# Performance work log

Measured on AMD Instinct MI355X. Metric: run time of the kernel, lower is better.

## Reference

```python
import jax, jax.numpy as jnp
import numpy as np

H = 4096          # hidden_size
NIN = 17          # RFSIZE*RFSIZE + ADDINPUT + NBACTIONS = 9+4+4
NA = 4            # NBACTIONS


def setup_inputs() -> dict:
    key = jax.random.key(0)
    ks = jax.random.split(key, 12)
    return {
        "x": jax.random.normal(ks[0], (1, NIN), jnp.float32),
        "hidden": 0.1 * jax.random.normal(ks[1], (1, H), jnp.float32),
        "hebb": 0.01 * jax.random.normal(ks[2], (H, H), jnp.float32),
        "i2h_w": 0.1 * jax.random.normal(ks[3], (H, NIN), jnp.float32),
        "i2h_b": 0.1 * jax.random.normal(ks[4], (H,), jnp.float32),
        "w": 0.01 * jax.random.uniform(ks[5], (H, H), jnp.float32),
        "alpha": 0.01 * jax.random.uniform(ks[6], (H, H), jnp.float32),
        "eta": 0.01 * jnp.ones((1,), jnp.float32),
        "h2o_w": 0.1 * jax.random.normal(ks[7], (NA, H), jnp.float32),
        "h2o_b": 0.1 * jax.random.normal(ks[8], (NA,), jnp.float32),
        "h2v_w": 0.1 * jax.random.normal(ks[9], (1, H), jnp.float32),
        "h2v_b": 0.1 * jax.random.normal(ks[10], (1,), jnp.float32),
    }


def reference(x, hidden, hebb, i2h_w, i2h_b, w, alpha, eta, h2o_w, h2o_b, h2v_w, h2v_b):
    # plastic RNN step: h = tanh(i2h(x) + hidden @ (w + alpha*hebb))
    h = jnp.tanh(x @ i2h_w.T + i2h_b + hidden @ (w + alpha * hebb))  # [1,H]
    # Hebbian trace update: (1-eta)*hebb + eta * outer(hidden, h)
    hebb_new = (1.0 - eta) * hebb + eta * (hidden[0][:, None] * h[0][None, :])  # [H,H]
    activout = jax.nn.softmax(h @ h2o_w.T + h2o_b, axis=-1)  # [1,NA]
    valueout = h @ h2v_w.T + h2v_b                           # [1,1]
    return activout, valueout, h, hebb_new
```

## Files before the change

### kernel.cpp

```cpp
#include <hip/hip_runtime.h>

#define HDIM 4096
#define NIN 17
#define NA 4

constexpr int TB = 256;
constexpr int CPT = 4;
constexpr int BXC = HDIM / (TB * CPT);
constexpr int NCHUNK = 256;
constexpr int RPC = HDIM / NCHUNK;

__global__ __launch_bounds__(TB)
void k_matvec(const float* __restrict__ w, const float* __restrict__ alpha,
              const float* __restrict__ hebb, const float* __restrict__ hidden,
              float* __restrict__ partial) {
    const int col0 = (blockIdx.x * TB + threadIdx.x) * CPT;
    const int row0 = blockIdx.y * RPC;
    float4 acc = make_float4(0.f, 0.f, 0.f, 0.f);
#pragma unroll 4
    for (int r = 0; r < RPC; ++r) {
        const int i = row0 + r;
        const size_t off = (size_t)i * HDIM + col0;
        const float hv = hidden[i];
        const float4 wv = *(const float4*)(w + off);
        const float4 av = *(const float4*)(alpha + off);
        const float4 bv = *(const float4*)(hebb + off);
        acc.x += hv * (wv.x + av.x * bv.x);
        acc.y += hv * (wv.y + av.y * bv.y);
        acc.z += hv * (wv.z + av.z * bv.z);
        acc.w += hv * (wv.w + av.w * bv.w);
    }
    *(float4*)(partial + (size_t)blockIdx.y * HDIM + col0) = acc;
}

__global__ __launch_bounds__(256)
void k_hact(const float* __restrict__ partial,
            const float* __restrict__ x, const float* __restrict__ i2h_w,
            const float* __restrict__ i2h_b,
            float* __restrict__ h_f, float* __restrict__ h_out) {
    const int j = blockIdx.x * 256 + threadIdx.x;
    float s = 0.f;
    for (int c = 0; c < NCHUNK; ++c) s += partial[(size_t)c * HDIM + j];
    float z = i2h_b[j] + s;
#pragma unroll
    for (int k = 0; k < NIN; ++k) z += x[k] * i2h_w[j * NIN + k];
    const float h = tanhf(z);
    h_f[j] = h;
    h_out[j] = h;
}

__global__ __launch_bounds__(256)
void k_hebb(const float* __restrict__ hebb, const float* __restrict__ hidden,
            const float* __restrict__ h_f, const float* __restrict__ eta,
            float* __restrict__ hebb_out) {
    const size_t m = ((size_t)blockIdx.x * 256 + threadIdx.x) * 4;
    const float e = eta[0];
    const float om = 1.f - e;
    const int i = (int)(m >> 12);
    const int j = (int)(m & (HDIM - 1));
    const float hv = e * hidden[i];
    const float4 hb = *(const float4*)(hebb + m);
    const float4 hj = *(const float4*)(h_f + j);
    hebb_out[m]     = om * hb.x + hv * hj.x;
    hebb_out[m + 1] = om * hb.y + hv * hj.y;
    hebb_out[m + 2] = om * hb.z + hv * hj.z;
    hebb_out[m + 3] = om * hb.w + hv * hj.w;
}

__global__ __launch_bounds__(256)
void k_heads(const float* __restrict__ h_f,
             const float* __restrict__ h2o_w, const float* __restrict__ h2o_b,
             const float* __restrict__ h2v_w, const float* __restrict__ h2v_b,
             float* __restrict__ out) {
    const int tid = threadIdx.x;
    float acc[NA + 1] = {0.f, 0.f, 0.f, 0.f, 0.f};
    for (int t = 0; t < HDIM / 256; ++t) {
        const int j = t * 256 + tid;
        const float hv = h_f[j];
#pragma unroll
        for (int a = 0; a < NA; ++a) acc[a] += hv * h2o_w[a * HDIM + j];
        acc[NA] += hv * h2v_w[j];
    }
    __shared__ float red[256];
    __shared__ float res[NA + 1];
    for (int a = 0; a < NA + 1; ++a) {
        red[tid] = acc[a];
        __syncthreads();
        for (int sft = 128; sft > 0; sft >>= 1) {
            if (tid < sft) red[tid] += red[tid + sft];
            __syncthreads();
        }
        if (tid == 0) res[a] = red[0];
        __syncthreads();
    }
    if (tid == 0) {
        float o[NA];
        float mx = -1e30f;
        for (int a = 0; a < NA; ++a) { o[a] = res[a] + h2o_b[a]; mx = fmaxf(mx, o[a]); }
        float se = 0.f;
        for (int a = 0; a < NA; ++a) { o[a] = __expf(o[a] - mx); se += o[a]; }
        for (int a = 0; a < NA; ++a) out[a] = o[a] / se;
        out[NA] = res[NA] + h2v_b[0];
    }
}

extern "C" void kernel_launch(void* const* d_in, const int* in_sizes, int n_in,
                              void* d_out, int out_size, void* d_ws, size_t ws_size,
                              hipStream_t stream) {
    const float* x      = (const float*)d_in[0];
    const float* hidden = (const float*)d_in[1];
    const float* hebb   = (const float*)d_in[2];
    const float* i2h_w  = (const float*)d_in[3];
    const float* i2h_b  = (const float*)d_in[4];
    const float* w      = (const float*)d_in[5];
    const float* alpha  = (const float*)d_in[6];
    const float* eta    = (const float*)d_in[7];
    const float* h2o_w  = (const float*)d_in[8];
    const float* h2o_b  = (const float*)d_in[9];
    const float* h2v_w  = (const float*)d_in[10];
    const float* h2v_b  = (const float*)d_in[11];
    float* out = (float*)d_out;

    float* partial = (float*)d_ws;
    float* h_f = partial + (size_t)NCHUNK * HDIM;

    float* h_out    = out + 5;
    float* hebb_out = out + 5 + HDIM;

    k_matvec<<<dim3(BXC, NCHUNK), TB, 0, stream>>>(w, alpha, hebb, hidden, partial);
    k_hact<<<HDIM / 256, 256, 0, stream>>>(partial, x, i2h_w, i2h_b, h_f, h_out);
    k_hebb<<<(int)(((size_t)HDIM * HDIM) / 1024), 256, 0, stream>>>(hebb, hidden, h_f, eta, hebb_out);
    k_heads<<<1, 256, 0, stream>>>(h_f, h2o_w, h2o_b, h2v_w, h2v_b, out);
}
```

Baseline: 270.1 us.

## Replace partial-sum buffer with atomic reduction and fuse heads into activation kernel

The matvec kernel now accumulates column sums straight into a zeroed workspace vector with float atomics, replacing the per-chunk partial buffer and its serial reduction over 256 chunks in k_hact. The chunk count doubles to 512, the inner loop is fully unrolled, and a min-blocks-per-CU launch bound is added. The output heads are computed inside k_hact with wavefront shuffles and atomics, so the single-block heads kernel is replaced by a tiny finish kernel. This trades the write and read of a 4 MB partial buffer for 2M atomic adds plus an extra init launch, and the float summation order becomes nondeterministic.

```diff
diff --git a/kernel.cpp b/kernel.cpp
--- a/kernel.cpp
+++ b/kernel.cpp
@@ -7,17 +7,27 @@
 constexpr int TB = 256;
 constexpr int CPT = 4;
 constexpr int BXC = HDIM / (TB * CPT);
-constexpr int NCHUNK = 256;
+constexpr int NCHUNK = 512;
 constexpr int RPC = HDIM / NCHUNK;
 
-__global__ __launch_bounds__(TB)
+#define WS_Z 0
+#define WS_RES 4096
+#define WS_HF 4104
+
+__global__ __launch_bounds__(256)
+void k_init(float* __restrict__ ws) {
+    const int i = blockIdx.x * 256 + threadIdx.x;
+    if (i < WS_HF) ws[i] = 0.f;
+}
+
+__global__ __launch_bounds__(TB, 4)
 void k_matvec(const float* __restrict__ w, const float* __restrict__ alpha,
               const float* __restrict__ hebb, const float* __restrict__ hidden,
-              float* __restrict__ partial) {
+              float* __restrict__ z) {
     const int col0 = (blockIdx.x * TB + threadIdx.x) * CPT;
     const int row0 = blockIdx.y * RPC;
     float4 acc = make_float4(0.f, 0.f, 0.f, 0.f);
-#pragma unroll 4
+#pragma unroll
     for (int r = 0; r < RPC; ++r) {
         const int i = row0 + r;
         const size_t off = (size_t)i * HDIM + col0;
@@ -30,23 +40,57 @@
         acc.z += hv * (wv.z + av.z * bv.z);
         acc.w += hv * (wv.w + av.w * bv.w);
     }
-    *(float4*)(partial + (size_t)blockIdx.y * HDIM + col0) = acc;
+    atomicAdd(z + col0 + 0, acc.x);
+    atomicAdd(z + col0 + 1, acc.y);
+    atomicAdd(z + col0 + 2, acc.z);
+    atomicAdd(z + col0 + 3, acc.w);
 }
 
 __global__ __launch_bounds__(256)
-void k_hact(const float* __restrict__ partial,
+void k_hact(const float* __restrict__ z,
             const float* __restrict__ x, const float* __restrict__ i2h_w,
             const float* __restrict__ i2h_b,
-            float* __restrict__ h_f, float* __restrict__ h_out) {
+            const float* __restrict__ h2o_w, const float* __restrict__ h2v_w,
+            float* __restrict__ h_f, float* __restrict__ h_out,
+            float* __restrict__ res) {
     const int j = blockIdx.x * 256 + threadIdx.x;
-    float s = 0.f;
-    for (int c = 0; c < NCHUNK; ++c) s += partial[(size_t)c * HDIM + j];
-    float z = i2h_b[j] + s;
+    float zv = z[j] + i2h_b[j];
 #pragma unroll
-    for (int k = 0; k < NIN; ++k) z += x[k] * i2h_w[j * NIN + k];
-    const float h = tanhf(z);
+    for (int k = 0; k < NIN; ++k) zv += x[k] * i2h_w[j * NIN + k];
+    const float h = tanhf(zv);
     h_f[j] = h;
     h_out[j] = h;
+    float d[NA + 1];
+#pragma unroll
+    for (int a = 0; a < NA; ++a) d[a] = h * h2o_w[a * HDIM + j];
+    d[NA] = h * h2v_w[j];
+#pragma unroll
+    for (int a = 0; a < NA + 1; ++a) {
+#pragma unroll
+        for (int off = 32; off > 0; off >>= 1) d[a] += __shfl_down(d[a], off);
+    }
+    if ((threadIdx.x & 63) == 0) {
+#pragma unroll
+        for (int a = 0; a < NA + 1; ++a) atomicAdd(res + a, d[a]);
+    }
+}
+
+__global__ void k_finish(const float* __restrict__ res,
+                         const float* __restrict__ h2o_b,
+                         const float* __restrict__ h2v_b,
+                         float* __restrict__ out) {
+    if (threadIdx.x == 0) {
+        float o[NA];
+        float mx = -1e30f;
+#pragma unroll
+        for (int a = 0; a < NA; ++a) { o[a] = res[a] + h2o_b[a]; mx = fmaxf(mx, o[a]); }
+        float se = 0.f;
+#pragma unroll
+        for (int a = 0; a < NA; ++a) { o[a] = __expf(o[a] - mx); se += o[a]; }
+#pragma unroll
+        for (int a = 0; a < NA; ++a) out[a] = o[a] / se;
+        out[NA] = res[NA] + h2v_b[0];
+    }
 }
 
 __global__ __launch_bounds__(256)
@@ -67,43 +111,6 @@
     hebb_out[m + 3] = om * hb.w + hv * hj.w;
 }
 
-__global__ __launch_bounds__(256)
-void k_heads(const float* __restrict__ h_f,
-             const float* __restrict__ h2o_w, const float* __restrict__ h2o_b,
-             const float* __restrict__ h2v_w, const float* __restrict__ h2v_b,
-             float* __restrict__ out) {
-    const int tid = threadIdx.x;
-    float acc[NA + 1] = {0.f, 0.f, 0.f, 0.f, 0.f};
-    for (int t = 0; t < HDIM / 256; ++t) {
-        const int j = t * 256 + tid;
-        const float hv = h_f[j];
-#pragma unroll
-        for (int a = 0; a < NA; ++a) acc[a] += hv * h2o_w[a * HDIM + j];
-        acc[NA] += hv * h2v_w[j];
-    }
-    __shared__ float red[256];
-    __shared__ float res[NA + 1];
-    for (int a = 0; a < NA + 1; ++a) {
-        red[tid] = acc[a];
-        __syncthreads();
-        for (int sft = 128; sft > 0; sft >>= 1) {
-            if (tid < sft) red[tid] += red[tid + sft];
-            __syncthreads();
-        }
-        if (tid == 0) res[a] = red[0];
-        __syncthreads();
-    }
-    if (tid == 0) {
-        float o[NA];
-        float mx = -1e30f;
-        for (int a = 0; a < NA; ++a) { o[a] = res[a] + h2o_b[a]; mx = fmaxf(mx, o[a]); }
-        float se = 0.f;
-        for (int a = 0; a < NA; ++a) { o[a] = __expf(o[a] - mx); se += o[a]; }
-        for (int a = 0; a < NA; ++a) out[a] = o[a] / se;
-        out[NA] = res[NA] + h2v_b[0];
-    }
-}
-
 extern "C" void kernel_launch(void* const* d_in, const int* in_sizes, int n_in,
                               void* d_out, int out_size, void* d_ws, size_t ws_size,
                               hipStream_t stream) {
@@ -121,14 +128,17 @@
     const float* h2v_b  = (const float*)d_in[11];
     float* out = (float*)d_out;
 
-    float* partial = (float*)d_ws;
-    float* h_f = partial + (size_t)NCHUNK * HDIM;
+    float* ws  = (float*)d_ws;
+    float* z   = ws + WS_Z;
+    float* res = ws + WS_RES;
+    float* h_f = ws + WS_HF;
 
     float* h_out    = out + 5;
     float* hebb_out = out + 5 + HDIM;
 
-    k_matvec<<<dim3(BXC, NCHUNK), TB, 0, stream>>>(w, alpha, hebb, hidden, partial);
-    k_hact<<<HDIM / 256, 256, 0, stream>>>(partial, x, i2h_w, i2h_b, h_f, h_out);
+    k_init<<<(WS_HF + 255) / 256, 256, 0, stream>>>(ws);
+    k_matvec<<<dim3(BXC, NCHUNK), TB, 0, stream>>>(w, alpha, hebb, hidden, z);
+    k_hact<<<HDIM / 256, 256, 0, stream>>>(z, x, i2h_w, i2h_b, h2o_w, h2v_w, h_f, h_out, res);
+    k_finish<<<1, 64, 0, stream>>>(res, h2o_b, h2v_b, out);
     k_hebb<<<(int)(((size_t)HDIM * HDIM) / 1024), 256, 0, stream>>>(hebb, hidden, h_f, eta, hebb_out);
-    k_heads<<<1, 256, 0, stream>>>(h_f, h2o_w, h2o_b, h2v_w, h2v_b, out);
 }
```

Result: no change. 272.2 us (+0.8%).
